# Performance work log

Measured on AMD Instinct MI355X. Metric: run time of the kernel, lower is better.

Reference implementation:

```python
import jax, jax.numpy as jnp
import numpy as np

DIM = 1024
NUM_HEADS = 16
HEAD_DIM = DIM // NUM_HEADS
THETA = 10000.0


def apply_rope(x):
    # x: [B, S, H, D]; Llama-style interleaved rotary pairs.
    S, D = x.shape[1], x.shape[3]
    half = D // 2
    inv_freq = THETA ** (-jnp.arange(half, dtype=jnp.float32) * 2.0 / D)  # [D/2]
    angles = jnp.arange(S, dtype=jnp.float32)[:, None] * inv_freq[None, :]  # [S, D/2]
    cos = jnp.cos(angles)[None, :, None, :]  # [1,S,1,D/2]
    sin = jnp.sin(angles)[None, :, None, :]
    x_even = x[..., 0::2]
    x_odd = x[..., 1::2]
    out_even = x_even * cos - x_odd * sin
    out_odd = x_even * sin + x_odd * cos
    out = jnp.stack([out_even, out_odd], axis=-1).reshape(x.shape)
    return out.astype(x.dtype)


def setup_inputs() -> dict:
    key = jax.random.key(0)
    ks = jax.random.split(key, 5)
    B, S = 2, 2048
    x = jax.random.normal(ks[0], (B, S, DIM), dtype=jnp.float32)
    scale = 1.0 / np.sqrt(DIM)
    Wq = jax.random.normal(ks[1], (DIM, DIM), dtype=jnp.float32) * scale
    Wk = jax.random.normal(ks[2], (DIM, DIM), dtype=jnp.float32) * scale
    Wv = jax.random.normal(ks[3], (DIM, DIM), dtype=jnp.float32) * scale
    Wo = jax.random.normal(ks[4], (DIM, DIM), dtype=jnp.float32) * scale
    return {"x": x, "Wq": Wq, "Wk": Wk, "Wv": Wv, "Wo": Wo}


def reference(x, Wq, Wk, Wv, Wo):
    B, S, _ = x.shape
    # torch Linear: y = x @ W^T
    q = (x @ Wq.T).reshape(B, S, NUM_HEADS, HEAD_DIM)
    k = (x @ Wk.T).reshape(B, S, NUM_HEADS, HEAD_DIM)
    v = (x @ Wv.T).reshape(B, S, NUM_HEADS, HEAD_DIM)
    q = apply_rope(q)
    k = apply_rope(k)
    # causal SDPA, scale = 1/sqrt(head_dim)
    scale = 1.0 / np.sqrt(HEAD_DIM).astype(np.float32)
    scores = jnp.einsum("bqhd,bkhd->bhqk", q, k) * scale  # [B,H,S,S]
    causal = jnp.tril(jnp.ones((S, S), dtype=bool))
    scores = jnp.where(causal[None, None], scores, jnp.finfo(scores.dtype).min)
    attn = jax.nn.softmax(scores, axis=-1)
    y = jnp.einsum("bhqk,bkhd->bqhd", attn, v).reshape(B, S, DIM)
    return y @ Wo.T
```

## Files before the change

kernel.cpp:

```cpp
#include <hip/hip_runtime.h>
#include <hip/hip_bf16.h>

typedef __attribute__((ext_vector_type(8))) __bf16 bf16x8;
typedef __attribute__((ext_vector_type(4))) __bf16 bf16x4;
typedef __attribute__((ext_vector_type(4))) float f32x4;

#define DIM 1024
#define SLEN 2048
#define NH 16
#define HD 64

__device__ __forceinline__ f32x4 MFMA(bf16x8 a, bf16x8 b, f32x4 c) {
    return __builtin_amdgcn_mfma_f32_16x16x32_bf16(a, b, c, 0, 0, 0);
}

__global__ __launch_bounds__(256) void cvt_bf16(const float* __restrict__ in,
                                                __bf16* __restrict__ out, int n) {
    int i = (blockIdx.x * blockDim.x + threadIdx.x) * 8;
    if (i >= n) return;
    f32x4 a = *reinterpret_cast<const f32x4*>(in + i);
    f32x4 b = *reinterpret_cast<const f32x4*>(in + i + 4);
    bf16x8 o;
#pragma unroll
    for (int j = 0; j < 4; ++j) { o[j] = (__bf16)a[j]; o[j + 4] = (__bf16)b[j]; }
    *reinterpret_cast<bf16x8*>(out + i) = o;
}

__global__ __launch_bounds__(256) void cvt_w4(const float* __restrict__ w0,
                                              const float* __restrict__ w1,
                                              const float* __restrict__ w2,
                                              const float* __restrict__ w3,
                                              __bf16* __restrict__ o0,
                                              __bf16* __restrict__ o1,
                                              __bf16* __restrict__ o2,
                                              __bf16* __restrict__ o3) {
    int s = blockIdx.y;
    const float* in = s == 0 ? w0 : s == 1 ? w1 : s == 2 ? w2 : w3;
    __bf16* out = s == 0 ? o0 : s == 1 ? o1 : s == 2 ? o2 : o3;
    int i = (blockIdx.x * blockDim.x + threadIdx.x) * 8;
    f32x4 a = *reinterpret_cast<const f32x4*>(in + i);
    f32x4 b = *reinterpret_cast<const f32x4*>(in + i + 4);
    bf16x8 o;
#pragma unroll
    for (int j = 0; j < 4; ++j) { o[j] = (__bf16)a[j]; o[j + 4] = (__bf16)b[j]; }
    *reinterpret_cast<bf16x8*>(out + i) = o;
}

__global__ __launch_bounds__(256) void rope2(__bf16* __restrict__ q,
                                             __bf16* __restrict__ k) {
    __bf16* t = blockIdx.y == 0 ? q : k;
    const float scale = blockIdx.y == 0 ? 0.18033688011112042f : 1.0f;
    int idx = blockIdx.x * blockDim.x + threadIdx.x;
    int row = idx >> 9;
    int p = idx & 511;
    int head = p >> 5;
    int j = p & 31;
    int s = row & (SLEN - 1);
    float inv = expf(-0.28782313662425574f * (float)j);
    float angle = (float)s * inv;
    float sn, cs;
    sincosf(angle, &sn, &cs);
    size_t base = (size_t)row * DIM + head * HD + 2 * j;
    float e = (float)t[base], o = (float)t[base + 1];
    t[base] = (__bf16)((e * cs - o * sn) * scale);
    t[base + 1] = (__bf16)((e * sn + o * cs) * scale);
}

__global__ __launch_bounds__(256) void gemm_qkv(const __bf16* __restrict__ X,
                                                const __bf16* __restrict__ Wq,
                                                const __bf16* __restrict__ Wk,
                                                const __bf16* __restrict__ Wv,
                                                __bf16* __restrict__ Qo,
                                                __bf16* __restrict__ Ko,
                                                __bf16* __restrict__ Vt) {
    __shared__ alignas(16) __bf16 Alds[128 * 64];
    __shared__ alignas(16) __bf16 Blds[128 * 64];
    const int tid = threadIdx.x;
    const int lane = tid & 63;
    const int w = tid >> 6;
    const int wr = w >> 1, wc = w & 1;
    const int l15 = lane & 15, lhi = lane >> 4;
    const int l7 = l15 & 7;
    const int m0 = blockIdx.y * 128;
    const int n0g = blockIdx.x * 128;
    const int seg = n0g >> 10;
    const int n0 = n0g & 1023;
    const __bf16* __restrict__ B = seg == 0 ? Wq : seg == 1 ? Wk : Wv;
    const int K = 1024, N = 1024;

    const int lrow = lane >> 3;
    const int scol = ((lane & 7) ^ lrow) * 8;

    f32x4 acc[4][4] = {};

    for (int kt = 0; kt < K; kt += 64) {
#pragma unroll
        for (int c = 0; c < 4; ++c) {
            int r0 = c * 32 + w * 8;
            const __bf16* sa = &X[(size_t)(m0 + r0 + lrow) * K + kt + scol];
            const __bf16* sb = &B[(size_t)(n0 + r0 + lrow) * K + kt + scol];
            __builtin_amdgcn_global_load_lds((const __attribute__((address_space(1))) void*)sa,
                                             (__attribute__((address_space(3))) void*)&Alds[r0 * 64],
                                             16, 0, 0);
            __builtin_amdgcn_global_load_lds((const __attribute__((address_space(1))) void*)sb,
                                             (__attribute__((address_space(3))) void*)&Blds[r0 * 64],
                                             16, 0, 0);
        }
        __syncthreads();
#pragma unroll
        for (int kk = 0; kk < 2; ++kk) {
            bf16x8 af[4], bfr[4];
#pragma unroll
            for (int i = 0; i < 4; ++i) {
                af[i] = *(const bf16x8*)&Alds[(wr * 64 + i * 16 + l15) * 64 + 8 * ((kk * 4 + lhi) ^ l7)];
                bfr[i] = *(const bf16x8*)&Blds[(wc * 64 + i * 16 + l15) * 64 + 8 * ((kk * 4 + lhi) ^ l7)];
            }
            __builtin_amdgcn_s_setprio(1);
#pragma unroll
            for (int i = 0; i < 4; ++i)
#pragma unroll
                for (int j = 0; j < 4; ++j)
                    acc[i][j] = MFMA(af[i], bfr[j], acc[i][j]);
            __builtin_amdgcn_s_setprio(0);
        }
        __syncthreads();
    }
    if (seg < 2) {
        __bf16* __restrict__ O = seg == 0 ? Qo : Ko;
#pragma unroll
        for (int i = 0; i < 4; ++i)
#pragma unroll
            for (int j = 0; j < 4; ++j)
#pragma unroll
                for (int r = 0; r < 4; ++r) {
                    int row = m0 + wr * 64 + i * 16 + lhi * 4 + r;
                    int col = n0 + wc * 64 + j * 16 + l15;
                    O[(size_t)row * N + col] = (__bf16)acc[i][j][r];
                }
    } else {
#pragma unroll
        for (int i = 0; i < 4; ++i)
#pragma unroll
            for (int j = 0; j < 4; ++j) {
                int row = m0 + wr * 64 + i * 16 + lhi * 4;
                int col = n0 + wc * 64 + j * 16 + l15;
                int bb = row >> 11, s = row & 2047;
                int hh = col >> 6, d = col & 63;
                bf16x4 pk;
#pragma unroll
                for (int r = 0; r < 4; ++r) pk[r] = (__bf16)acc[i][j][r];
                *(bf16x4*)&Vt[((size_t)(bb * 16 + hh) * 64 + d) * SLEN + s] = pk;
            }
    }
}

__global__ __launch_bounds__(256) void gemm_o(const __bf16* __restrict__ A,
                                              const __bf16* __restrict__ B,
                                              float* __restrict__ C) {
    __shared__ alignas(16) __bf16 Alds[64 * 64];
    __shared__ alignas(16) __bf16 Blds[128 * 64];
    const int tid = threadIdx.x;
    const int lane = tid & 63;
    const int w = tid >> 6;
    const int wr = w >> 1, wc = w & 1;
    const int l15 = lane & 15, lhi = lane >> 4;
    const int l7 = l15 & 7;
    const int m0 = blockIdx.y * 64;
    const int n0 = blockIdx.x * 128;
    const int K = 1024, N = 1024;

    const int lrow = lane >> 3;
    const int scol = ((lane & 7) ^ lrow) * 8;

    f32x4 acc[2][4] = {};

    for (int kt = 0; kt < K; kt += 64) {
#pragma unroll
        for (int c = 0; c < 2; ++c) {
            int r0 = c * 32 + w * 8;
            const __bf16* sa = &A[(size_t)(m0 + r0 + lrow) * K + kt + scol];
            __builtin_amdgcn_global_load_lds((const __attribute__((address_space(1))) void*)sa,
                                             (__attribute__((address_space(3))) void*)&Alds[r0 * 64],
                                             16, 0, 0);
        }
#pragma unroll
        for (int c = 0; c < 4; ++c) {
            int r0 = c * 32 + w * 8;
            const __bf16* sb = &B[(size_t)(n0 + r0 + lrow) * K + kt + scol];
            __builtin_amdgcn_global_load_lds((const __attribute__((address_space(1))) void*)sb,
                                             (__attribute__((address_space(3))) void*)&Blds[r0 * 64],
                                             16, 0, 0);
        }
        __syncthreads();
#pragma unroll
        for (int kk = 0; kk < 2; ++kk) {
            bf16x8 af[2], bfr[4];
#pragma unroll
            for (int i = 0; i < 2; ++i)
                af[i] = *(const bf16x8*)&Alds[(wr * 32 + i * 16 + l15) * 64 + 8 * ((kk * 4 + lhi) ^ l7)];
#pragma unroll
            for (int j = 0; j < 4; ++j)
                bfr[j] = *(const bf16x8*)&Blds[(wc * 64 + j * 16 + l15) * 64 + 8 * ((kk * 4 + lhi) ^ l7)];
            __builtin_amdgcn_s_setprio(1);
#pragma unroll
            for (int i = 0; i < 2; ++i)
#pragma unroll
                for (int j = 0; j < 4; ++j)
                    acc[i][j] = MFMA(af[i], bfr[j], acc[i][j]);
            __builtin_amdgcn_s_setprio(0);
        }
        __syncthreads();
    }
#pragma unroll
    for (int i = 0; i < 2; ++i)
#pragma unroll
        for (int j = 0; j < 4; ++j)
#pragma unroll
            for (int r = 0; r < 4; ++r) {
                int row = m0 + wr * 32 + i * 16 + lhi * 4 + r;
                int col = n0 + wc * 64 + j * 16 + l15;
                C[(size_t)row * N + col] = acc[i][j][r];
            }
}

__global__ __launch_bounds__(256, 4) void attn_kernel(const __bf16* __restrict__ Q,
                                                      const __bf16* __restrict__ K,
                                                      const __bf16* __restrict__ Vt,
                                                      __bf16* __restrict__ Y) {
    __shared__ __bf16 Klds[2][64 * 64];
    __shared__ __bf16 Vlds[2][64 * 64];
    __shared__ __bf16 Plds[4][16][64];

    const int tid = threadIdx.x;
    const int lane = tid & 63;
    const int w = tid >> 6;
    const int l15 = lane & 15, lhi = lane >> 4;
    const int l7 = l15 & 7;
    const int l14 = l15 & 14;

    const int id = blockIdx.x;
    const int x = id & 7, j = id >> 3;
    const int qt = 31 - (j >> 2);
    const int bh = 4 * x + (j & 3);
    const int b = bh >> 4, h = bh & 15;

    const int srow = lane >> 3;
    const int scs = (lane & 7) ^ srow;

    const __bf16* skA = K + (size_t)b * SLEN * DIM + h * HD + (size_t)(8 * w + srow) * DIM + scs * 8;
    const __bf16* skB = skA + 32 * DIM;
    const __bf16* svA = Vt + (size_t)bh * 64 * SLEN + (size_t)(8 * w + srow) * SLEN + scs * 8;
    const __bf16* svB = svA + 32 * SLEN;
    const int dA = (8 * w + srow) * 64;
    const int dB = dA + 32 * 64;

    int koffs[4][2], voffs[2][4], pw[4];
#pragma unroll
    for (int nb = 0; nb < 4; ++nb) {
        koffs[nb][0] = (nb * 16 + l15) * 64 + 8 * (lhi ^ l7);
        koffs[nb][1] = (nb * 16 + l15) * 64 + 8 * ((4 + lhi) ^ l7);
        pw[nb] = ((nb * 4 + lhi) ^ l14) * 4;
    }
#pragma unroll
    for (int kk = 0; kk < 2; ++kk)
#pragma unroll
        for (int nd = 0; nd < 4; ++nd)
            voffs[kk][nd] = (nd * 16 + l15) * 64 + 8 * ((kk * 4 + lhi) ^ l7);
    const int pr0 = ((lhi * 2) ^ l14) * 4;
    const int pr1 = ((8 + lhi * 2) ^ l14) * 4;
    __bf16* Pme = &Plds[w][l15][0];

    const int qrow_g = qt * 64 + w * 16 + l15;
    const size_t qbase = (size_t)(b * SLEN + qrow_g) * DIM + h * HD;
    const bf16x8 qf0 = *(const bf16x8*)&Q[qbase + lhi * 8];
    const bf16x8 qf1 = *(const bf16x8*)&Q[qbase + 32 + lhi * 8];

    bf16x8 ones;
#pragma unroll
    for (int t = 0; t < 8; ++t) ones[t] = (__bf16)1.0f;

    f32x4 acc[4] = {};
    f32x4 accL = {};

    auto stage = [&](int buf) {
        __builtin_amdgcn_global_load_lds((const __attribute__((address_space(1))) void*)skA,
                                         (__attribute__((address_space(3))) void*)&Klds[buf][dA], 16, 0, 0);
        __builtin_amdgcn_global_load_lds((const __attribute__((address_space(1))) void*)skB,
                                         (__attribute__((address_space(3))) void*)&Klds[buf][dB], 16, 0, 0);
        __builtin_amdgcn_global_load_lds((const __attribute__((address_space(1))) void*)svA,
                                         (__attribute__((address_space(3))) void*)&Vlds[buf][dA], 16, 0, 0);
        __builtin_amdgcn_global_load_lds((const __attribute__((address_space(1))) void*)svB,
                                         (__attribute__((address_space(3))) void*)&Vlds[buf][dB], 16, 0, 0);
        skA += 64 * DIM; skB += 64 * DIM;
        svA += 64; svB += 64;
    };

    const int nkt = qt + 1;
    stage(0);
    for (int kt = 0; kt < nkt; ++kt) {
        const int cur = kt & 1;
        __syncthreads();
        if (kt + 1 < nkt) stage(cur ^ 1);
        const __bf16* Kc = Klds[cur];
        const __bf16* Vc = Vlds[cur];

        f32x4 sT[4];
        __builtin_amdgcn_s_setprio(1);
#pragma unroll
        for (int nb = 0; nb < 4; ++nb) {
            bf16x8 k0 = *(const bf16x8*)&Kc[koffs[nb][0]];
            bf16x8 k1 = *(const bf16x8*)&Kc[koffs[nb][1]];
            f32x4 a = {};
            a = MFMA(k0, qf0, a);
            a = MFMA(k1, qf1, a);
            sT[nb] = a;
        }
        __builtin_amdgcn_s_setprio(0);
        if (kt == qt) {
#pragma unroll
            for (int nb = 0; nb < 4; ++nb)
#pragma unroll
                for (int r = 0; r < 4; ++r)
                    if (nb * 16 + lhi * 4 + r > w * 16 + l15) sT[nb][r] = -1e30f;
        }
#pragma unroll
        for (int nb = 0; nb < 4; ++nb) {
            bf16x4 pk;
#pragma unroll
            for (int r = 0; r < 4; ++r) pk[r] = (__bf16)exp2f(sT[nb][r] - 16.0f);
            *(bf16x4*)&Pme[pw[nb]] = pk;
        }

        __builtin_amdgcn_s_setprio(1);
        const bf16x8 pf0 = *(const bf16x8*)&Pme[pr0];
        const bf16x8 pf1 = *(const bf16x8*)&Pme[pr1];
        accL = MFMA(ones, pf0, accL);
        accL = MFMA(ones, pf1, accL);
#pragma unroll
        for (int nd = 0; nd < 4; ++nd) {
            acc[nd] = MFMA(*(const bf16x8*)&Vc[voffs[0][nd]], pf0, acc[nd]);
            acc[nd] = MFMA(*(const bf16x8*)&Vc[voffs[1][nd]], pf1, acc[nd]);
        }
        __builtin_amdgcn_s_setprio(0);
    }
    const float inv = 1.0f / accL[0];
#pragma unroll
    for (int nd = 0; nd < 4; ++nd) {
        bf16x4 o;
#pragma unroll
        for (int r = 0; r < 4; ++r) o[r] = (__bf16)(acc[nd][r] * inv);
        *(bf16x4*)&Y[(size_t)(b * SLEN + qrow_g) * DIM + h * HD + nd * 16 + lhi * 4] = o;
    }
}

extern "C" void kernel_launch(void* const* d_in, const int* in_sizes, int n_in,
                              void* d_out, int out_size, void* d_ws, size_t ws_size,
                              hipStream_t stream) {
    const float* x = (const float*)d_in[0];
    const float* Wq = (const float*)d_in[1];
    const float* Wk = (const float*)d_in[2];
    const float* Wv = (const float*)d_in[3];
    const float* Wo = (const float*)d_in[4];
    float* out = (float*)d_out;

    const size_t XN = (size_t)4096 * 1024;
    const size_t WN = (size_t)1024 * 1024;

    __bf16* xb = (__bf16*)d_ws;
    __bf16* qb = xb + XN;
    __bf16* kb = qb + XN;
    __bf16* vtb = kb + XN;
    __bf16* wqb = vtb + XN;
    __bf16* wkb = wqb + WN;
    __bf16* wvb = wkb + WN;
    __bf16* wob = wvb + WN;
    __bf16* yb = xb;

    cvt_bf16<<<XN / 8 / 256, 256, 0, stream>>>(x, xb, (int)XN);
    dim3 gw(WN / 8 / 256, 4);
    cvt_w4<<<gw, 256, 0, stream>>>(Wq, Wk, Wv, Wo, wqb, wkb, wvb, wob);

    dim3 gq(24, 32);
    gemm_qkv<<<gq, 256, 0, stream>>>(xb, wqb, wkb, wvb, qb, kb, vtb);

    int pairs = 4096 * (DIM / 2);
    dim3 gr(pairs / 256, 2);
    rope2<<<gr, 256, 0, stream>>>(qb, kb);

    attn_kernel<<<1024, 256, 0, stream>>>(qb, kb, vtb, yb);

    dim3 go(8, 64);
    gemm_o<<<go, 256, 0, stream>>>(yb, wob, out);
}
```

Baseline: 112.5 us.

## Switch attention to 32x32 MFMA with split-K waves and register P exchange

Rewrites the attention inner loop to use 32x32x16 bf16 MFMA. Each wave owns a 32-query by 32-key quadrant, and the two key halves are reduced through LDS at the end. P is rebuilt in registers with permlane32_swap instead of a round trip through LDS. The row sum is taken with scalar adds rather than a ones-MFMA. This drops the P LDS traffic and MFMA instruction count, at the cost of an extra cross-wave reduction and more live registers.

```diff
diff --git a/kernel.cpp b/kernel.cpp
--- a/kernel.cpp
+++ b/kernel.cpp
@@ -4,6 +4,9 @@
 typedef __attribute__((ext_vector_type(8))) __bf16 bf16x8;
 typedef __attribute__((ext_vector_type(4))) __bf16 bf16x4;
 typedef __attribute__((ext_vector_type(4))) float f32x4;
+typedef __attribute__((ext_vector_type(16))) float f32x16;
+typedef __attribute__((ext_vector_type(2))) unsigned int uint2v;
+typedef __attribute__((ext_vector_type(4))) unsigned int uint4v;
 
 #define DIM 1024
 #define SLEN 2048
@@ -12,6 +15,14 @@
 
 __device__ __forceinline__ f32x4 MFMA(bf16x8 a, bf16x8 b, f32x4 c) {
     return __builtin_amdgcn_mfma_f32_16x16x32_bf16(a, b, c, 0, 0, 0);
+}
+__device__ __forceinline__ f32x16 MFMA32(bf16x8 a, bf16x8 b, f32x16 c) {
+    return __builtin_amdgcn_mfma_f32_32x32x16_bf16(a, b, c, 0, 0, 0);
+}
+__device__ __forceinline__ unsigned pack_bf16(float a, float b) {
+    unsigned short ua = __builtin_bit_cast(unsigned short, (__bf16)a);
+    unsigned short ub = __builtin_bit_cast(unsigned short, (__bf16)b);
+    return ((unsigned)ub << 16) | (unsigned)ua;
 }
 
 __global__ __launch_bounds__(256) void cvt_bf16(const float* __restrict__ in,
@@ -229,71 +240,62 @@
                                                       __bf16* __restrict__ Y) {
     __shared__ __bf16 Klds[2][64 * 64];
     __shared__ __bf16 Vlds[2][64 * 64];
-    __shared__ __bf16 Plds[4][16][64];
 
     const int tid = threadIdx.x;
     const int lane = tid & 63;
     const int w = tid >> 6;
-    const int l15 = lane & 15, lhi = lane >> 4;
-    const int l7 = l15 & 7;
-    const int l14 = l15 & 14;
+    const int qhalf = w & 1, khalf = w >> 1;
+    const int l31 = lane & 31;
+    const int hi32 = lane >> 5;
+    const int l7 = l31 & 7;
 
     const int id = blockIdx.x;
-    const int x = id & 7, j = id >> 3;
-    const int qt = 31 - (j >> 2);
-    const int bh = 4 * x + (j & 3);
+    const int x = id & 7, jj = id >> 3;
+    const int qt = 31 - (jj >> 2);
+    const int bh = 4 * x + (jj & 3);
     const int b = bh >> 4, h = bh & 15;
 
     const int srow = lane >> 3;
     const int scs = (lane & 7) ^ srow;
-
-    const __bf16* skA = K + (size_t)b * SLEN * DIM + h * HD + (size_t)(8 * w + srow) * DIM + scs * 8;
-    const __bf16* skB = skA + 32 * DIM;
-    const __bf16* svA = Vt + (size_t)bh * 64 * SLEN + (size_t)(8 * w + srow) * SLEN + scs * 8;
-    const __bf16* svB = svA + 32 * SLEN;
+    const __bf16* skP = K + (size_t)b * SLEN * DIM + h * HD + (size_t)(8 * w + srow) * DIM + scs * 8;
+    const __bf16* svP = Vt + (size_t)bh * 64 * SLEN + (size_t)(8 * w + srow) * SLEN + scs * 8;
     const int dA = (8 * w + srow) * 64;
-    const int dB = dA + 32 * 64;
-
-    int koffs[4][2], voffs[2][4], pw[4];
-#pragma unroll
-    for (int nb = 0; nb < 4; ++nb) {
-        koffs[nb][0] = (nb * 16 + l15) * 64 + 8 * (lhi ^ l7);
-        koffs[nb][1] = (nb * 16 + l15) * 64 + 8 * ((4 + lhi) ^ l7);
-        pw[nb] = ((nb * 4 + lhi) ^ l14) * 4;
-    }
-#pragma unroll
-    for (int kk = 0; kk < 2; ++kk)
-#pragma unroll
-        for (int nd = 0; nd < 4; ++nd)
-            voffs[kk][nd] = (nd * 16 + l15) * 64 + 8 * ((kk * 4 + lhi) ^ l7);
-    const int pr0 = ((lhi * 2) ^ l14) * 4;
-    const int pr1 = ((8 + lhi * 2) ^ l14) * 4;
-    __bf16* Pme = &Plds[w][l15][0];
-
-    const int qrow_g = qt * 64 + w * 16 + l15;
-    const size_t qbase = (size_t)(b * SLEN + qrow_g) * DIM + h * HD;
-    const bf16x8 qf0 = *(const bf16x8*)&Q[qbase + lhi * 8];
-    const bf16x8 qf1 = *(const bf16x8*)&Q[qbase + 32 + lhi * 8];
-
-    bf16x8 ones;
-#pragma unroll
-    for (int t = 0; t < 8; ++t) ones[t] = (__bf16)1.0f;
-
-    f32x4 acc[4] = {};
-    f32x4 accL = {};
 
     auto stage = [&](int buf) {
-        __builtin_amdgcn_global_load_lds((const __attribute__((address_space(1))) void*)skA,
-                                         (__attribute__((address_space(3))) void*)&Klds[buf][dA], 16, 0, 0);
-        __builtin_amdgcn_global_load_lds((const __attribute__((address_space(1))) void*)skB,
-                                         (__attribute__((address_space(3))) void*)&Klds[buf][dB], 16, 0, 0);
-        __builtin_amdgcn_global_load_lds((const __attribute__((address_space(1))) void*)svA,
-                                         (__attribute__((address_space(3))) void*)&Vlds[buf][dA], 16, 0, 0);
-        __builtin_amdgcn_global_load_lds((const __attribute__((address_space(1))) void*)svB,
-                                         (__attribute__((address_space(3))) void*)&Vlds[buf][dB], 16, 0, 0);
-        skA += 64 * DIM; skB += 64 * DIM;
-        svA += 64; svB += 64;
+#pragma unroll
+        for (int i = 0; i < 2; ++i) {
+            __builtin_amdgcn_global_load_lds(
+                (const __attribute__((address_space(1))) void*)(skP + (size_t)i * 32 * DIM),
+                (__attribute__((address_space(3))) void*)&Klds[buf][dA + i * 32 * 64], 16, 0, 0);
+            __builtin_amdgcn_global_load_lds(
+                (const __attribute__((address_space(1))) void*)(svP + (size_t)i * 32 * SLEN),
+                (__attribute__((address_space(3))) void*)&Vlds[buf][dA + i * 32 * 64], 16, 0, 0);
+        }
+        skP += 64 * DIM;
+        svP += 64;
     };
+
+    const int qloc = qhalf * 32 + l31;
+    const int qg = qt * 64 + qloc;
+    const size_t qbase = (size_t)(b * SLEN + qg) * DIM + h * HD;
+    bf16x8 qf0 = *(const bf16x8*)&Q[qbase + 0 + 8 * hi32];
+    bf16x8 qf1 = *(const bf16x8*)&Q[qbase + 16 + 8 * hi32];
+    bf16x8 qf2 = *(const bf16x8*)&Q[qbase + 32 + 8 * hi32];
+    bf16x8 qf3 = *(const bf16x8*)&Q[qbase + 48 + 8 * hi32];
+
+    const int krowbase = (khalf * 32 + l31) * 64;
+    const int koff0 = krowbase + 8 * ((0 + hi32) ^ l7);
+    const int koff1 = krowbase + 8 * ((2 + hi32) ^ l7);
+    const int koff2 = krowbase + 8 * ((4 + hi32) ^ l7);
+    const int koff3 = krowbase + 8 * ((6 + hi32) ^ l7);
+    const int vrow0 = l31 * 64, vrow1 = (32 + l31) * 64;
+    const int voff00 = vrow0 + 8 * ((4 * khalf + 0 + hi32) ^ l7);
+    const int voff01 = vrow0 + 8 * ((4 * khalf + 2 + hi32) ^ l7);
+    const int voff10 = vrow1 + 8 * ((4 * khalf + 0 + hi32) ^ l7);
+    const int voff11 = vrow1 + 8 * ((4 * khalf + 2 + hi32) ^ l7);
+
+    f32x16 acc0 = {}, acc1 = {};
+    float lsum = 0.f;
 
     const int nkt = qt + 1;
     stage(0);
@@ -304,52 +306,84 @@
         const __bf16* Kc = Klds[cur];
         const __bf16* Vc = Vlds[cur];
 
-        f32x4 sT[4];
+        f32x16 S = {};
         __builtin_amdgcn_s_setprio(1);
-#pragma unroll
-        for (int nb = 0; nb < 4; ++nb) {
-            bf16x8 k0 = *(const bf16x8*)&Kc[koffs[nb][0]];
-            bf16x8 k1 = *(const bf16x8*)&Kc[koffs[nb][1]];
-            f32x4 a = {};
-            a = MFMA(k0, qf0, a);
-            a = MFMA(k1, qf1, a);
-            sT[nb] = a;
-        }
+        S = MFMA32(*(const bf16x8*)&Kc[koff0], qf0, S);
+        S = MFMA32(*(const bf16x8*)&Kc[koff1], qf1, S);
+        S = MFMA32(*(const bf16x8*)&Kc[koff2], qf2, S);
+        S = MFMA32(*(const bf16x8*)&Kc[koff3], qf3, S);
         __builtin_amdgcn_s_setprio(0);
+
         if (kt == qt) {
 #pragma unroll
-            for (int nb = 0; nb < 4; ++nb)
-#pragma unroll
-                for (int r = 0; r < 4; ++r)
-                    if (nb * 16 + lhi * 4 + r > w * 16 + l15) sT[nb][r] = -1e30f;
-        }
-#pragma unroll
-        for (int nb = 0; nb < 4; ++nb) {
-            bf16x4 pk;
-#pragma unroll
-            for (int r = 0; r < 4; ++r) pk[r] = (__bf16)exp2f(sT[nb][r] - 16.0f);
-            *(bf16x4*)&Pme[pw[nb]] = pk;
+            for (int r = 0; r < 16; ++r) {
+                const int krow = (r & 3) + 8 * (r >> 2) + 4 * hi32 + 32 * khalf;
+                if (krow > qloc) S[r] = -1e30f;
+            }
+        }
+        float p[16];
+#pragma unroll
+        for (int r = 0; r < 16; ++r) p[r] = exp2f(S[r] - 16.0f);
+        float s0 = (p[0] + p[1]) + (p[2] + p[3]);
+        float s1 = (p[4] + p[5]) + (p[6] + p[7]);
+        float s2 = (p[8] + p[9]) + (p[10] + p[11]);
+        float s3 = (p[12] + p[13]) + (p[14] + p[15]);
+        lsum += (s0 + s1) + (s2 + s3);
+
+        bf16x8 pf[2];
+#pragma unroll
+        for (int ss = 0; ss < 2; ++ss) {
+            unsigned P01 = pack_bf16(p[8 * ss + 0], p[8 * ss + 1]);
+            unsigned P23 = pack_bf16(p[8 * ss + 2], p[8 * ss + 3]);
+            unsigned Q01 = pack_bf16(p[8 * ss + 4], p[8 * ss + 5]);
+            unsigned Q23 = pack_bf16(p[8 * ss + 6], p[8 * ss + 7]);
+            uint2v sa = __builtin_amdgcn_permlane32_swap(P01, Q01, false, false);
+            uint2v sb = __builtin_amdgcn_permlane32_swap(P23, Q23, false, false);
+            uint4v pwv = {sa[0], sb[0], sa[1], sb[1]};
+            pf[ss] = __builtin_bit_cast(bf16x8, pwv);
         }
 
         __builtin_amdgcn_s_setprio(1);
-        const bf16x8 pf0 = *(const bf16x8*)&Pme[pr0];
-        const bf16x8 pf1 = *(const bf16x8*)&Pme[pr1];
-        accL = MFMA(ones, pf0, accL);
-        accL = MFMA(ones, pf1, accL);
-#pragma unroll
-        for (int nd = 0; nd < 4; ++nd) {
-            acc[nd] = MFMA(*(const bf16x8*)&Vc[voffs[0][nd]], pf0, acc[nd]);
-            acc[nd] = MFMA(*(const bf16x8*)&Vc[voffs[1][nd]], pf1, acc[nd]);
-        }
+        acc0 = MFMA32(*(const bf16x8*)&Vc[voff00], pf[0], acc0);
+        acc0 = MFMA32(*(const bf16x8*)&Vc[voff01], pf[1], acc0);
+        acc1 = MFMA32(*(const bf16x8*)&Vc[voff10], pf[0], acc1);
+        acc1 = MFMA32(*(const bf16x8*)&Vc[voff11], pf[1], acc1);
         __builtin_amdgcn_s_setprio(0);
     }
-    const float inv = 1.0f / accL[0];
-#pragma unroll
-    for (int nd = 0; nd < 4; ++nd) {
-        bf16x4 o;
-#pragma unroll
-        for (int r = 0; r < 4; ++r) o[r] = (__bf16)(acc[nd][r] * inv);
-        *(bf16x4*)&Y[(size_t)(b * SLEN + qrow_g) * DIM + h * HD + nd * 16 + lhi * 4] = o;
+
+    float* fbuf = (float*)&Klds[0][0];
+    float* lbuf = (float*)&Vlds[0][0];
+    __syncthreads();
+    if (khalf == 1) {
+#pragma unroll
+        for (int r = 0; r < 16; ++r) {
+            fbuf[(qhalf * 2 + 0) * 1024 + r * 64 + lane] = acc0[r];
+            fbuf[(qhalf * 2 + 1) * 1024 + r * 64 + lane] = acc1[r];
+        }
+        lbuf[qhalf * 64 + lane] = lsum;
+    }
+    __syncthreads();
+    if (khalf == 0) {
+#pragma unroll
+        for (int r = 0; r < 16; ++r) {
+            acc0[r] += fbuf[(qhalf * 2 + 0) * 1024 + r * 64 + lane];
+            acc1[r] += fbuf[(qhalf * 2 + 1) * 1024 + r * 64 + lane];
+        }
+        lsum += lbuf[qhalf * 64 + lane];
+        lsum += __shfl_xor(lsum, 32);
+        const float inv = 1.0f / lsum;
+        const size_t obase = (size_t)(b * SLEN + qg) * DIM + h * HD;
+#pragma unroll
+        for (int g = 0; g < 4; ++g) {
+            bf16x4 o0, o1;
+#pragma unroll
+            for (int e = 0; e < 4; ++e) {
+                o0[e] = (__bf16)(acc0[g * 4 + e] * inv);
+                o1[e] = (__bf16)(acc1[g * 4 + e] * inv);
+            }
+            *(bf16x4*)&Y[obase + 8 * g + 4 * hi32] = o0;
+            *(bf16x4*)&Y[obase + 32 + 8 * g + 4 * hi32] = o1;
+        }
     }
 }
 
```

After: 111.1 us. No clear change (-1.2%).
